# Kernel optimization log

Measured on AMD Instinct MI355X. Metric: run time of the kernel, lower is better.

## Reference

```python
import jax, jax.numpy as jnp
import numpy as np
import math

B, L, DX, DH, DFF, N, M = 16, 1024, 2, 512, 2048, 3, 8
DK = DH // M  # 64
EPS = 1e-5


def batchnorm_pos(z):
    # fresh nn.BatchNorm1d(L, affine=False) in train mode on [B, L, DH]:
    # per-position (dim 1) mean/var over (batch, feature) axes, biased variance
    mu = jnp.mean(z, axis=(0, 2), keepdims=True)
    var = jnp.mean(jnp.square(z - mu), axis=(0, 2), keepdims=True)
    return (z - mu) / jnp.sqrt(var + EPS)


def setup_inputs() -> dict:
    key = jax.random.key(0)
    ks = jax.random.split(key, 13)
    s = lambda k, shape, scale: jax.random.normal(k, shape, dtype=jnp.float32) * scale
    return {
        "x": s(ks[0], (B, L, DX), 1.0),
        "Wh": s(ks[1], (DH, DX), 1.0 / math.sqrt(DX)),
        "bh": s(ks[2], (DH,), 0.02),
        "Wq": s(ks[3], (N, M, DK, DH), 1.0 / math.sqrt(DH)),
        "Wk": s(ks[4], (N, M, DK, DH), 1.0 / math.sqrt(DH)),
        "Wv": s(ks[5], (N, M, DK, DH), 1.0 / math.sqrt(DH)),
        "Wo": s(ks[6], (N, M, DH, DK), 1.0 / math.sqrt(DK)),
        "w_bn": s(ks[7], (N, DH), 1.0),
        "b_bn": s(ks[8], (N, DH), 1.0),
        "Wff0": s(ks[9], (N, DFF, DH), 1.0 / math.sqrt(DH)),
        "bff0": s(ks[10], (N, DFF), 0.02),
        "Wff1": s(ks[11], (N, DH, DFF), 1.0 / math.sqrt(DFF)),
        "bff1": s(ks[12], (N, DH), 0.02),
    }


def reference(x, Wh, bh, Wq, Wk, Wv, Wo, w_bn, b_bn, Wff0, bff0, Wff1, bff1):
    n_layers = Wq.shape[0]
    dk = Wq.shape[2]
    scale = 1.0 / math.sqrt(dk)
    h = jnp.einsum("bld,ed->ble", x, Wh) + bh  # [B, L, DH]
    for n in range(n_layers):
        # batched multi-head attention (replaces per-head python loop)
        q = jnp.einsum("bld,mkd->bmlk", h, Wq[n])  # [B, M, L, DK]
        k = jnp.einsum("bld,mkd->bmlk", h, Wk[n])
        v = jnp.einsum("bld,mvd->bmlv", h, Wv[n])
        scores = jnp.einsum("bmlk,bmjk->bmlj", q, k) * scale  # [B, M, L, L]
        attn = jax.nn.softmax(scores, axis=-1)
        t = jnp.einsum("bmlj,bmjv->bmlv", attn, v)
        h_mha = jnp.einsum("bmlv,mdv->bld", t, Wo[n])  # sum over heads
        h_bn = w_bn[n] * batchnorm_pos(h + h_mha) + b_bn[n]
        ff = jnp.einsum("blf,df->bld", jax.nn.relu(jnp.einsum("bld,fd->blf", h_bn, Wff0[n]) + bff0[n]), Wff1[n]) + bff1[n]
        h = w_bn[n] * batchnorm_pos(h_bn + ff) + b_bn[n]
    return h
```

## Files before the change

### kernel.cpp

```cpp
#include <hip/hip_runtime.h>
#include <hip/hip_bf16.h>
#include <math.h>

#define B_   16
#define L_   1024
#define BL_  16384
#define DH_  512
#define DFF_ 2048
#define NL_  3
#define M_   8
#define DK_  64

typedef __attribute__((ext_vector_type(8))) short bf16x8;
typedef __attribute__((ext_vector_type(4))) float f32x4;
typedef __attribute__((ext_vector_type(4))) unsigned short us4;
typedef __attribute__((ext_vector_type(8))) unsigned short us8;

__device__ __forceinline__ unsigned short f2b(float x) {
    __hip_bfloat16 h = __float2bfloat16(x);
    return *(unsigned short*)&h;
}
__device__ __forceinline__ float b2f(unsigned short u) {
    unsigned int v = ((unsigned int)u) << 16;
    return __builtin_bit_cast(float, v);
}

#define GLDS(g, l) __builtin_amdgcn_global_load_lds( \
        (const __attribute__((address_space(1))) unsigned int*)(const void*)(g), \
        (__attribute__((address_space(3))) unsigned int*)(void*)(l), 16, 0, 0)

#define QKV_T 2359296
#define WO_T  786432
#define FF_T  3145728
__global__ __launch_bounds__(256) void wprep_kernel(
    const float* __restrict__ Wq, const float* __restrict__ Wk,
    const float* __restrict__ Wv, const float* __restrict__ Wo,
    const float* __restrict__ Wff0, const float* __restrict__ Wff1,
    unsigned short* __restrict__ wqkvb3, unsigned short* __restrict__ wob3,
    unsigned short* __restrict__ wff0b3, unsigned short* __restrict__ wff1b3)
{
    int i4 = (blockIdx.x * 256 + threadIdx.x) * 4;
    const float* src;
    unsigned short* dst;
    if (i4 < QKV_T) {
        int n = i4 / 786432, r = i4 % 786432;
        if (r < 262144)      src = Wq + (size_t)n * 262144 + r;
        else if (r < 524288) src = Wk + (size_t)n * 262144 + r - 262144;
        else                 src = Wv + (size_t)n * 262144 + r - 524288;
        dst = wqkvb3 + i4;
    } else if (i4 < QKV_T + WO_T) {
        int i = i4 - QKV_T;
        int n = i / 262144, r = i % 262144;
        int d = r >> 9, mv = r & 511, mm = mv >> 6, vv = mv & 63;
        src = Wo + (size_t)n * 262144 + ((size_t)mm * 512 + d) * 64 + vv;
        dst = wob3 + i;
    } else if (i4 < QKV_T + WO_T + FF_T) {
        int i = i4 - QKV_T - WO_T;
        src = Wff0 + i;
        dst = wff0b3 + i;
    } else {
        int i = i4 - QKV_T - WO_T - FF_T;
        src = Wff1 + i;
        dst = wff1b3 + i;
    }
    float4 v = *(const float4*)src;
    us4 o;
    o.x = f2b(v.x); o.y = f2b(v.y); o.z = f2b(v.z); o.w = f2b(v.w);
    *(us4*)dst = o;
}

__global__ __launch_bounds__(256) void embed_kernel(
    const float* __restrict__ x, const float* __restrict__ Wh,
    const float* __restrict__ bh, unsigned short* __restrict__ hb)
{
    int idx = blockIdx.x * 256 + threadIdx.x;
    int bl = idx >> 7;
    int e0 = (idx & 127) * 4;
    float x0 = x[bl * 2], x1 = x[bl * 2 + 1];
    us4 o;
    #pragma unroll
    for (int r = 0; r < 4; ++r) {
        int e = e0 + r;
        float v = fmaf(x0, Wh[e * 2], fmaf(x1, Wh[e * 2 + 1], bh[e]));
        ((unsigned short*)&o)[r] = f2b(v);
    }
    *(us4*)&hb[(size_t)bl * DH_ + e0] = o;
}

template<int NF>
__global__ __launch_bounds__(512, 2) void gemm8p_kernel(
    const unsigned short* __restrict__ A, const unsigned short* __restrict__ Bm,
    const float* __restrict__ bias, unsigned short* __restrict__ Cb,
    unsigned short* __restrict__ vT, int K, int cn, int flags)
{
    constexpr int BN   = NF * 64;
    constexpr int SLOT = 32768 + BN * 128;
    __shared__ unsigned char lds[2 * SLOT];

    const int tid  = threadIdx.x;
    const int lane = tid & 63, wid = tid >> 6;
    const int wr = wid >> 2, wc = wid & 3;
    const int fr = lane & 15, fq = lane >> 4;
    const int bm0 = blockIdx.y * 256, bn0 = blockIdx.x * BN;
    const int cxor = (fr & 7) << 4;

    const int srow  = tid >> 3;
    const int scole = ((tid & 7) ^ (srow & 7)) * 8;
    const unsigned short* Ag = A  + (size_t)(bm0 + srow) * K + scole;
    const unsigned short* Bg = Bm + (size_t)(bn0 + srow) * K + scole;

    f32x4 acc[8][NF];
    #pragma unroll
    for (int i = 0; i < 8; ++i)
        #pragma unroll
        for (int j = 0; j < NF; ++j)
            acc[i][j] = (f32x4){0.f, 0.f, 0.f, 0.f};

    auto ldsA = [&](int slot, int sweep) -> void* {
        return (void*)(lds + slot * SLOT + sweep * 8192 + wid * 1024);
    };
    auto ldsB = [&](int slot, int sweep) -> void* {
        return (void*)(lds + slot * SLOT + 32768 + sweep * 8192 + wid * 1024);
    };
    auto srcA = [&](int kt, int sweep) {
        return Ag + (size_t)sweep * 64 * K + kt * 64;
    };
    auto srcB = [&](int kt, int sweep) {
        return Bg + (size_t)sweep * 64 * K + kt * 64;
    };

    const int nt = K >> 6;

    if constexpr (NF == 4) {
        GLDS(srcB(0, 0), ldsB(0, 0)); GLDS(srcB(0, 1), ldsB(0, 1));
        GLDS(srcB(0, 2), ldsB(0, 2)); GLDS(srcB(0, 3), ldsB(0, 3));
    } else {
        GLDS(srcB(0, 0), ldsB(0, 0)); GLDS(srcB(0, 1), ldsB(0, 1));
    }
    GLDS(srcA(0, 0), ldsA(0, 0)); GLDS(srcA(0, 2), ldsA(0, 2));
    GLDS(srcA(0, 1), ldsA(0, 1)); GLDS(srcA(0, 3), ldsA(0, 3));
    asm volatile("s_waitcnt vmcnt(2)" ::: "memory");
    __builtin_amdgcn_s_barrier();

    for (int kt = 0; kt < nt; ++kt) {
        const int slot = kt & 1;
        const unsigned char* sb = lds + slot * SLOT;
        const int ns = slot ^ 1;
        const bool stg = (kt + 1 < nt);
        const int kn = kt + 1;

#define PHASE(P)                                                               \
    {                                                                          \
        constexpr int mh = (P) >> 1, nh = (P) & 1;                             \
        bf16x8 af[4][2], bfr[NF / 2][2];                                       \
        _Pragma("unroll")                                                      \
        for (int mi = 0; mi < 4; ++mi)                                         \
            _Pragma("unroll")                                                  \
            for (int kk = 0; kk < 2; ++kk)                                     \
                af[mi][kk] = *(const bf16x8*)(sb +                             \
                    (wr * 128 + mh * 64 + mi * 16 + fr) * 128 +                \
                    ((kk * 64 + fq * 16) ^ cxor));                             \
        _Pragma("unroll")                                                      \
        for (int ni = 0; ni < NF / 2; ++ni)                                    \
            _Pragma("unroll")                                                  \
            for (int kk = 0; kk < 2; ++kk)                                     \
                bfr[ni][kk] = *(const bf16x8*)(sb + 32768 +                    \
                    (wc * NF * 16 + nh * (NF / 2) * 16 + ni * 16 + fr) * 128 + \
                    ((kk * 64 + fq * 16) ^ cxor));                             \
        if (stg) {                                                             \
            if constexpr (NF == 4) {                                           \
                if ((P) == 0) { GLDS(srcB(kn, 0), ldsB(ns, 0));                \
                                GLDS(srcB(kn, 1), ldsB(ns, 1)); }              \
                if ((P) == 1) { GLDS(srcB(kn, 2), ldsB(ns, 2));                \
                                GLDS(srcB(kn, 3), ldsB(ns, 3)); }              \
                if ((P) == 2) { GLDS(srcA(kn, 0), ldsA(ns, 0));                \
                                GLDS(srcA(kn, 2), ldsA(ns, 2)); }              \
                if ((P) == 3) { GLDS(srcA(kn, 1), ldsA(ns, 1));                \
                                GLDS(srcA(kn, 3), ldsA(ns, 3)); }              \
            } else {                                                           \
                if ((P) == 0) { GLDS(srcB(kn, 0), ldsB(ns, 0));                \
                                GLDS(srcB(kn, 1), ldsB(ns, 1)); }              \
                if ((P) == 1) { GLDS(srcA(kn, 0), ldsA(ns, 0));                \
                                GLDS(srcA(kn, 2), ldsA(ns, 2)); }              \
                if ((P) == 2) { GLDS(srcA(kn, 1), ldsA(ns, 1));                \
                                GLDS(srcA(kn, 3), ldsA(ns, 3)); }              \
            }                                                                  \
        }                                                                      \
        if ((P) == 1) {                                                        \
            if (stg) asm volatile("s_waitcnt vmcnt(4)" ::: "memory");          \
            else     asm volatile("s_waitcnt vmcnt(0)" ::: "memory");          \
        }                                                                      \
        if ((P) == 3 && stg) asm volatile("s_waitcnt vmcnt(2)" ::: "memory");  \
        __builtin_amdgcn_s_barrier();                                          \
        asm volatile("s_waitcnt lgkmcnt(0)" ::: "memory");                     \
        __builtin_amdgcn_s_setprio(1);                                         \
        _Pragma("unroll")                                                      \
        for (int mi = 0; mi < 4; ++mi)                                         \
            _Pragma("unroll")                                                  \
            for (int ni = 0; ni < NF / 2; ++ni) {                              \
                f32x4 c = acc[mh * 4 + mi][nh * (NF / 2) + ni];                \
                c = __builtin_amdgcn_mfma_f32_16x16x32_bf16(                   \
                        af[mi][0], bfr[ni][0], c, 0, 0, 0);                    \
                c = __builtin_amdgcn_mfma_f32_16x16x32_bf16(                   \
                        af[mi][1], bfr[ni][1], c, 0, 0, 0);                    \
                acc[mh * 4 + mi][nh * (NF / 2) + ni] = c;                      \
            }                                                                  \
        __builtin_amdgcn_s_setprio(0);                                         \
        __builtin_amdgcn_s_barrier();                                          \
    }
        PHASE(0) PHASE(1) PHASE(2) PHASE(3)
#undef PHASE
    }

    float bj[NF];
    #pragma unroll
    for (int an = 0; an < NF; ++an) bj[an] = 0.f;
    if (flags & 1) {
        #pragma unroll
        for (int an = 0; an < NF; ++an)
            bj[an] = bias[bn0 + wc * NF * 16 + an * 16 + fr];
    }
    bool relu = flags & 2;
    bool qkvm = flags & 4;
    #pragma unroll
    for (int am = 0; am < 8; ++am) {
        int row0 = bm0 + wr * 128 + (am >> 2) * 64 + (am & 3) * 16 + fq * 4;
        #pragma unroll
        for (int an = 0; an < NF; ++an) {
            int col = bn0 + wc * NF * 16 + an * 16 + fr;
            float v[4];
            #pragma unroll
            for (int r = 0; r < 4; ++r) {
                v[r] = acc[am][an][r] + bj[an];
                if (relu) v[r] = fmaxf(v[r], 0.f);
            }
            if (qkvm) {
                if (col < 1024) {
                    float sc = (col < 512) ? 0.1803368801111244f : 1.0f;
                    #pragma unroll
                    for (int r = 0; r < 4; ++r)
                        Cb[(size_t)(row0 + r) * cn + col] = f2b(v[r] * sc);
                } else {
                    int mm = (col - 1024) >> 6, dd = (col - 1024) & 63;
                    int bb = row0 >> 10, l0 = row0 & 1023;
                    us4 p;
                    p.x = f2b(v[0]); p.y = f2b(v[1]); p.z = f2b(v[2]); p.w = f2b(v[3]);
                    *(us4*)&vT[((size_t)(bb * 8 + mm) * 64 + dd) * 1024 + l0] = p;
                }
            } else {
                #pragma unroll
                for (int r = 0; r < 4; ++r)
                    Cb[(size_t)(row0 + r) * cn + col] = f2b(v[r]);
            }
        }
    }
}

#define KST 72
__global__ __launch_bounds__(256, 4) void attn_mfma_kernel(
    const unsigned short* __restrict__ qk, const unsigned short* __restrict__ vT,
    unsigned short* __restrict__ t)
{
    __shared__ unsigned short Ks[64 * KST];
    __shared__ unsigned short Vs[64 * KST];
    __shared__ unsigned short Pb[4][32 * KST];

    int tid = threadIdx.x;
    int lane = tid & 63, wid = tid >> 6;
    int fr = lane & 15, fq = lane >> 4;
    int j = blockIdx.x;
    int pair = (j & 7) * 16 + (j >> 6);
    int q0 = ((j >> 3) & 7) * 128;
    int b = pair >> 3, m = pair & 7;
    int bq = b * L_;

    size_t qbase = (size_t)(bq + q0 + wid * 32) * 1024 + m * 64;
    bf16x8 qa[2][2];
    #pragma unroll
    for (int qh = 0; qh < 2; ++qh) {
        qa[qh][0] = *(const bf16x8*)&qk[qbase + (size_t)(qh * 16 + fr) * 1024 + fq * 8];
        qa[qh][1] = *(const bf16x8*)&qk[qbase + (size_t)(qh * 16 + fr) * 1024 + 32 + fq * 8];
    }

    f32x4 oacc[2][4];
    #pragma unroll
    for (int qh = 0; qh < 2; ++qh)
        #pragma unroll
        for (int i = 0; i < 4; ++i) oacc[qh][i] = (f32x4){0.f, 0.f, 0.f, 0.f};
    float lsum[2][4] = {{0.f, 0.f, 0.f, 0.f}, {0.f, 0.f, 0.f, 0.f}};

    int srow = tid >> 3;
    int scol = (tid & 7) * 8;
    const unsigned short* kg = qk + (size_t)bq * 1024 + 512 + m * 64 + scol;
    const unsigned short* vg = vT + ((size_t)pair * 64) * 1024 + scol;
    unsigned short* pw = Pb[wid];

    uint4 k0 = *(const uint4*)&kg[(size_t)(srow) * 1024];
    uint4 k1 = *(const uint4*)&kg[(size_t)(srow + 32) * 1024];
    uint4 v0 = *(const uint4*)&vg[(size_t)(srow) * 1024];
    uint4 v1 = *(const uint4*)&vg[(size_t)(srow + 32) * 1024];

    for (int kt = 0; kt < L_ / 64; ++kt) {
        __syncthreads();
        *(uint4*)&Ks[(srow)      * KST + scol] = k0;
        *(uint4*)&Ks[(srow + 32) * KST + scol] = k1;
        *(uint4*)&Vs[(srow)      * KST + scol] = v0;
        *(uint4*)&Vs[(srow + 32) * KST + scol] = v1;
        __syncthreads();
        if (kt + 1 < L_ / 64) {
            int kb = (kt + 1) * 64;
            k0 = *(const uint4*)&kg[(size_t)(kb + srow) * 1024];
            k1 = *(const uint4*)&kg[(size_t)(kb + srow + 32) * 1024];
            v0 = *(const uint4*)&vg[(size_t)(srow) * 1024 + kb];
            v1 = *(const uint4*)&vg[(size_t)(srow + 32) * 1024 + kb];
        }

        __builtin_amdgcn_s_setprio(1);
        #pragma unroll
        for (int nk = 0; nk < 4; ++nk) {
            bf16x8 kf0 = *(const bf16x8*)&Ks[(nk * 16 + fr) * KST + fq * 8];
            bf16x8 kf1 = *(const bf16x8*)&Ks[(nk * 16 + fr) * KST + 32 + fq * 8];
            #pragma unroll
            for (int qh = 0; qh < 2; ++qh) {
                f32x4 s = __builtin_amdgcn_mfma_f32_16x16x32_bf16(
                    qa[qh][0], kf0, (f32x4){0.f, 0.f, 0.f, 0.f}, 0, 0, 0);
                s = __builtin_amdgcn_mfma_f32_16x16x32_bf16(qa[qh][1], kf1, s, 0, 0, 0);
                #pragma unroll
                for (int r = 0; r < 4; ++r) {
                    float p = exp2f(s[r]);
                    lsum[qh][r] += p;
                    pw[(qh * 16 + fq * 4 + r) * KST + nk * 16 + fr] = f2b(p);
                }
            }
        }
        bf16x8 pa[2][2];
        #pragma unroll
        for (int qh = 0; qh < 2; ++qh) {
            pa[qh][0] = *(const bf16x8*)&pw[(qh * 16 + fr) * KST + fq * 8];
            pa[qh][1] = *(const bf16x8*)&pw[(qh * 16 + fr) * KST + 32 + fq * 8];
        }
        #pragma unroll
        for (int nt = 0; nt < 4; ++nt) {
            bf16x8 vf0 = *(const bf16x8*)&Vs[(nt * 16 + fr) * KST + fq * 8];
            bf16x8 vf1 = *(const bf16x8*)&Vs[(nt * 16 + fr) * KST + 32 + fq * 8];
            #pragma unroll
            for (int qh = 0; qh < 2; ++qh) {
                oacc[qh][nt] = __builtin_amdgcn_mfma_f32_16x16x32_bf16(
                    pa[qh][0], vf0, oacc[qh][nt], 0, 0, 0);
                oacc[qh][nt] = __builtin_amdgcn_mfma_f32_16x16x32_bf16(
                    pa[qh][1], vf1, oacc[qh][nt], 0, 0, 0);
            }
        }
        __builtin_amdgcn_s_setprio(0);
    }

    #pragma unroll
    for (int qh = 0; qh < 2; ++qh)
        #pragma unroll
        for (int r = 0; r < 4; ++r) {
            float s = lsum[qh][r];
            s += __shfl_xor(s, 1); s += __shfl_xor(s, 2);
            s += __shfl_xor(s, 4); s += __shfl_xor(s, 8);
            lsum[qh][r] = 1.f / s;
        }
    #pragma unroll
    for (int qh = 0; qh < 2; ++qh)
        #pragma unroll
        for (int r = 0; r < 4; ++r) {
            size_t orow = (size_t)(bq + q0 + wid * 32 + qh * 16 + fq * 4 + r) * DH_ + m * 64;
            #pragma unroll
            for (int nt = 0; nt < 4; ++nt)
                t[orow + nt * 16 + fr] = f2b(oacc[qh][nt][r] * lsum[qh][r]);
        }
}

__global__ __launch_bounds__(256) void bn_stats_kernel(
    const unsigned short* __restrict__ a, const unsigned short* __restrict__ b,
    float* __restrict__ stats)
{
    int l = blockIdx.x, tid = threadIdx.x;
    float s = 0.f, s2 = 0.f;
    #pragma unroll
    for (int u = tid; u < 1024; u += 256) {
        int bb = u >> 6, dg = (u & 63) * 8;
        size_t off = ((size_t)bb * L_ + l) * DH_ + dg;
        us8 va = *(const us8*)&a[off];
        us8 vb = *(const us8*)&b[off];
        #pragma unroll
        for (int j = 0; j < 8; ++j) {
            float z = b2f(va[j]) + b2f(vb[j]);
            s += z;
            s2 = fmaf(z, z, s2);
        }
    }
    #pragma unroll
    for (int off = 32; off > 0; off >>= 1) {
        s  += __shfl_down(s, off);
        s2 += __shfl_down(s2, off);
    }
    __shared__ float red[8];
    int w = tid >> 6;
    if ((tid & 63) == 0) { red[w] = s; red[4 + w] = s2; }
    __syncthreads();
    if (tid == 0) {
        float S  = red[0] + red[1] + red[2] + red[3];
        float S2 = red[4] + red[5] + red[6] + red[7];
        float mu  = S * (1.f / 8192.f);
        float var = S2 * (1.f / 8192.f) - mu * mu;
        stats[l]      = mu;
        stats[L_ + l] = rsqrtf(var + 1e-5f);
    }
}

__global__ __launch_bounds__(256) void bn_apply_kernel(
    const unsigned short* __restrict__ a, const unsigned short* __restrict__ b,
    const float* __restrict__ stats, const float* __restrict__ w,
    const float* __restrict__ bias, unsigned short* __restrict__ outb,
    float* __restrict__ outf)
{
    int idx = blockIdx.x * 256 + threadIdx.x;
    int bl = idx >> 6;
    int d0 = (idx & 63) * 8;
    int l  = bl & (L_ - 1);
    float mu = stats[l], rs = stats[L_ + l];
    size_t off = (size_t)bl * DH_ + d0;
    us8 va = *(const us8*)&a[off];
    us8 vb = *(const us8*)&b[off];
    float o[8];
    #pragma unroll
    for (int j = 0; j < 8; ++j) {
        float z = b2f(va[j]) + b2f(vb[j]);
        o[j] = fmaf(w[d0 + j], (z - mu) * rs, bias[d0 + j]);
    }
    if (outb) {
        us8 ob;
        #pragma unroll
        for (int j = 0; j < 8; ++j) ob[j] = f2b(o[j]);
        *(us8*)&outb[off] = ob;
    }
    if (outf) {
        float4 o0 = {o[0], o[1], o[2], o[3]};
        float4 o1 = {o[4], o[5], o[6], o[7]};
        *(float4*)&outf[off]     = o0;
        *(float4*)&outf[off + 4] = o1;
    }
}

extern "C" void kernel_launch(void* const* d_in, const int* in_sizes, int n_in,
                              void* d_out, int out_size, void* d_ws, size_t ws_size,
                              hipStream_t stream)
{
    const float* x    = (const float*)d_in[0];
    const float* Wh   = (const float*)d_in[1];
    const float* bh   = (const float*)d_in[2];
    const float* Wq   = (const float*)d_in[3];
    const float* Wk   = (const float*)d_in[4];
    const float* Wv   = (const float*)d_in[5];
    const float* Wo   = (const float*)d_in[6];
    const float* wbn  = (const float*)d_in[7];
    const float* bbn  = (const float*)d_in[8];
    const float* Wff0 = (const float*)d_in[9];
    const float* bff0 = (const float*)d_in[10];
    const float* Wff1 = (const float*)d_in[11];
    const float* bff1 = (const float*)d_in[12];
    float* out = (float*)d_out;

    float* st = (float*)d_ws;
    unsigned short* hb    = (unsigned short*)(st + 2048);
    unsigned short* qkkb  = hb + (size_t)BL_ * DH_;
    unsigned short* vTb   = qkkb + (size_t)BL_ * 1024;
    unsigned short* tb    = vTb + (size_t)BL_ * DH_;
    unsigned short* mhab  = tb + (size_t)BL_ * DH_;
    unsigned short* hbnb  = mhab + (size_t)BL_ * DH_;
    unsigned short* ffob  = hbnb + (size_t)BL_ * DH_;
    unsigned short* wqkvb3 = ffob + (size_t)BL_ * DH_;
    unsigned short* wob3   = wqkvb3 + QKV_T;
    unsigned short* wff0b3 = wob3 + WO_T;
    unsigned short* wff1b3 = wff0b3 + FF_T;
    unsigned short* ffmb  = qkkb;

    wprep_kernel<<<(QKV_T + WO_T + 2 * FF_T) / 1024, 256, 0, stream>>>(
        Wq, Wk, Wv, Wo, Wff0, Wff1, wqkvb3, wob3, wff0b3, wff1b3);
    embed_kernel<<<BL_ * DH_ / 4 / 256, 256, 0, stream>>>(x, Wh, bh, hb);

    dim3 gqkv(1536 / 128, BL_ / 256);
    dim3 gwo(512 / 128, BL_ / 256);
    dim3 gff0(2048 / 256, BL_ / 256);
    dim3 gff1(512 / 128, BL_ / 256);
    int gbn = BL_ * DH_ / 8 / 256;

    for (int n = 0; n < NL_; ++n) {
        const unsigned short* wqkvb = wqkvb3 + (size_t)n * 786432;
        const unsigned short* wob   = wob3   + (size_t)n * 262144;
        const unsigned short* wff0b = wff0b3 + (size_t)n * 1048576;
        const unsigned short* wff1b = wff1b3 + (size_t)n * 1048576;
        const float* wbn_n  = wbn  + (size_t)n * DH_;
        const float* bbn_n  = bbn  + (size_t)n * DH_;
        const float* bff0_n = bff0 + (size_t)n * DFF_;
        const float* bff1_n = bff1 + (size_t)n * DH_;
        bool last = (n == NL_ - 1);

        gemm8p_kernel<2><<<gqkv, 512, 0, stream>>>(hb, wqkvb, nullptr,
            qkkb, vTb, DH_, 1024, 4);
        attn_mfma_kernel<<<1024, 256, 0, stream>>>(qkkb, vTb, tb);
        gemm8p_kernel<2><<<gwo, 512, 0, stream>>>(tb, wob, nullptr,
            mhab, nullptr, DH_, DH_, 0);
        bn_stats_kernel<<<L_, 256, 0, stream>>>(hb, mhab, st);
        bn_apply_kernel<<<gbn, 256, 0, stream>>>(hb, mhab, st, wbn_n, bbn_n,
            hbnb, nullptr);
        gemm8p_kernel<4><<<gff0, 512, 0, stream>>>(hbnb, wff0b, bff0_n,
            ffmb, nullptr, DH_, DFF_, 1 | 2);
        gemm8p_kernel<2><<<gff1, 512, 0, stream>>>(ffmb, wff1b, bff1_n,
            ffob, nullptr, DFF_, DH_, 1);
        bn_stats_kernel<<<L_, 256, 0, stream>>>(hbnb, ffob, st);
        bn_apply_kernel<<<gbn, 256, 0, stream>>>(hbnb, ffob, st, wbn_n, bbn_n,
            last ? nullptr : hb, last ? out : nullptr);
    }
}
```

Measured before the change: 776.2 us.

## Swizzle GEMM workgroup order across XCDs and use two-phase loop for NF=2

Launches the GEMMs on a flat 1D grid and remaps each workgroup id so consecutive tiles land on the same XCD (chunked by 8). This improves L2 reuse of A and B tiles within each XCD. For NF=2 it also replaces the four-phase inner loop, whose last phases issued no loads, with a two-phase loop that spreads the next-tile global-to-LDS copies over both phases and adjusts the vmcnt waits to match. The remap relies on the grid size being divisible by 8, and the new wait counts must stay consistent with the issue order.

```diff
diff --git a/kernel.cpp b/kernel.cpp
--- a/kernel.cpp
+++ b/kernel.cpp
@@ -91,7 +91,7 @@
 __global__ __launch_bounds__(512, 2) void gemm8p_kernel(
     const unsigned short* __restrict__ A, const unsigned short* __restrict__ Bm,
     const float* __restrict__ bias, unsigned short* __restrict__ Cb,
-    unsigned short* __restrict__ vT, int K, int cn, int flags)
+    unsigned short* __restrict__ vT, int K, int cn, int flags, int gx)
 {
     constexpr int BN   = NF * 64;
     constexpr int SLOT = 32768 + BN * 128;
@@ -101,7 +101,14 @@
     const int lane = tid & 63, wid = tid >> 6;
     const int wr = wid >> 2, wc = wid & 3;
     const int fr = lane & 15, fq = lane >> 4;
-    const int bm0 = blockIdx.y * 256, bn0 = blockIdx.x * BN;
+
+    const int nwg = gridDim.x;
+    const int cpx = nwg >> 3;
+    const int wg  = blockIdx.x;
+    const int swz = (wg & 7) * cpx + (wg >> 3);
+    const int by  = swz / gx;
+    const int bx  = swz - by * gx;
+    const int bm0 = by * 256, bn0 = bx * BN;
     const int cxor = (fr & 7) << 4;
 
     const int srow  = tid >> 3;
@@ -149,10 +156,10 @@
         const bool stg = (kt + 1 < nt);
         const int kn = kt + 1;
 
-#define PHASE(P)                                                               \
+#define PHASE4(P)                                                              \
     {                                                                          \
         constexpr int mh = (P) >> 1, nh = (P) & 1;                             \
-        bf16x8 af[4][2], bfr[NF / 2][2];                                       \
+        bf16x8 af[4][2], bfr[2][2];                                            \
         _Pragma("unroll")                                                      \
         for (int mi = 0; mi < 4; ++mi)                                         \
             _Pragma("unroll")                                                  \
@@ -161,30 +168,21 @@
                     (wr * 128 + mh * 64 + mi * 16 + fr) * 128 +                \
                     ((kk * 64 + fq * 16) ^ cxor));                             \
         _Pragma("unroll")                                                      \
-        for (int ni = 0; ni < NF / 2; ++ni)                                    \
+        for (int ni = 0; ni < 2; ++ni)                                         \
             _Pragma("unroll")                                                  \
             for (int kk = 0; kk < 2; ++kk)                                     \
                 bfr[ni][kk] = *(const bf16x8*)(sb + 32768 +                    \
-                    (wc * NF * 16 + nh * (NF / 2) * 16 + ni * 16 + fr) * 128 + \
+                    (wc * 64 + nh * 32 + ni * 16 + fr) * 128 +                 \
                     ((kk * 64 + fq * 16) ^ cxor));                             \
         if (stg) {                                                             \
-            if constexpr (NF == 4) {                                           \
-                if ((P) == 0) { GLDS(srcB(kn, 0), ldsB(ns, 0));                \
-                                GLDS(srcB(kn, 1), ldsB(ns, 1)); }              \
-                if ((P) == 1) { GLDS(srcB(kn, 2), ldsB(ns, 2));                \
-                                GLDS(srcB(kn, 3), ldsB(ns, 3)); }              \
-                if ((P) == 2) { GLDS(srcA(kn, 0), ldsA(ns, 0));                \
-                                GLDS(srcA(kn, 2), ldsA(ns, 2)); }              \
-                if ((P) == 3) { GLDS(srcA(kn, 1), ldsA(ns, 1));                \
-                                GLDS(srcA(kn, 3), ldsA(ns, 3)); }              \
-            } else {                                                           \
-                if ((P) == 0) { GLDS(srcB(kn, 0), ldsB(ns, 0));                \
-                                GLDS(srcB(kn, 1), ldsB(ns, 1)); }              \
-                if ((P) == 1) { GLDS(srcA(kn, 0), ldsA(ns, 0));                \
-                                GLDS(srcA(kn, 2), ldsA(ns, 2)); }              \
-                if ((P) == 2) { GLDS(srcA(kn, 1), ldsA(ns, 1));                \
-                                GLDS(srcA(kn, 3), ldsA(ns, 3)); }              \
-            }                                                                  \
+            if ((P) == 0) { GLDS(srcB(kn, 0), ldsB(ns, 0));                    \
+                            GLDS(srcB(kn, 1), ldsB(ns, 1)); }                  \
+            if ((P) == 1) { GLDS(srcB(kn, 2), ldsB(ns, 2));                    \
+                            GLDS(srcB(kn, 3), ldsB(ns, 3)); }                  \
+            if ((P) == 2) { GLDS(srcA(kn, 0), ldsA(ns, 0));                    \
+                            GLDS(srcA(kn, 2), ldsA(ns, 2)); }                  \
+            if ((P) == 3) { GLDS(srcA(kn, 1), ldsA(ns, 1));                    \
+                            GLDS(srcA(kn, 3), ldsA(ns, 3)); }                  \
         }                                                                      \
         if ((P) == 1) {                                                        \
             if (stg) asm volatile("s_waitcnt vmcnt(4)" ::: "memory");          \
@@ -197,19 +195,74 @@
         _Pragma("unroll")                                                      \
         for (int mi = 0; mi < 4; ++mi)                                         \
             _Pragma("unroll")                                                  \
-            for (int ni = 0; ni < NF / 2; ++ni) {                              \
-                f32x4 c = acc[mh * 4 + mi][nh * (NF / 2) + ni];                \
+            for (int ni = 0; ni < 2; ++ni) {                                   \
+                f32x4 c = acc[mh * 4 + mi][nh * 2 + ni];                       \
                 c = __builtin_amdgcn_mfma_f32_16x16x32_bf16(                   \
                         af[mi][0], bfr[ni][0], c, 0, 0, 0);                    \
                 c = __builtin_amdgcn_mfma_f32_16x16x32_bf16(                   \
                         af[mi][1], bfr[ni][1], c, 0, 0, 0);                    \
-                acc[mh * 4 + mi][nh * (NF / 2) + ni] = c;                      \
+                acc[mh * 4 + mi][nh * 2 + ni] = c;                             \
             }                                                                  \
         __builtin_amdgcn_s_setprio(0);                                         \
         __builtin_amdgcn_s_barrier();                                          \
     }
-        PHASE(0) PHASE(1) PHASE(2) PHASE(3)
-#undef PHASE
+
+#define PHASE2(P)                                                              \
+    {                                                                          \
+        constexpr int mh = (P);                                                \
+        bf16x8 af[4][2], bfr[2][2];                                            \
+        _Pragma("unroll")                                                      \
+        for (int mi = 0; mi < 4; ++mi)                                         \
+            _Pragma("unroll")                                                  \
+            for (int kk = 0; kk < 2; ++kk)                                     \
+                af[mi][kk] = *(const bf16x8*)(sb +                             \
+                    (wr * 128 + mh * 64 + mi * 16 + fr) * 128 +                \
+                    ((kk * 64 + fq * 16) ^ cxor));                             \
+        _Pragma("unroll")                                                      \
+        for (int ni = 0; ni < 2; ++ni)                                         \
+            _Pragma("unroll")                                                  \
+            for (int kk = 0; kk < 2; ++kk)                                     \
+                bfr[ni][kk] = *(const bf16x8*)(sb + 32768 +                    \
+                    (wc * 32 + ni * 16 + fr) * 128 +                           \
+                    ((kk * 64 + fq * 16) ^ cxor));                             \
+        if (stg) {                                                             \
+            if ((P) == 0) { GLDS(srcB(kn, 0), ldsB(ns, 0));                    \
+                            GLDS(srcB(kn, 1), ldsB(ns, 1));                    \
+                            GLDS(srcA(kn, 0), ldsA(ns, 0)); }                  \
+            if ((P) == 1) { GLDS(srcA(kn, 2), ldsA(ns, 2));                    \
+                            GLDS(srcA(kn, 1), ldsA(ns, 1));                    \
+                            GLDS(srcA(kn, 3), ldsA(ns, 3)); }                  \
+        }                                                                      \
+        if ((P) == 0) {                                                        \
+            if (stg) asm volatile("s_waitcnt vmcnt(3)" ::: "memory");          \
+            else     asm volatile("s_waitcnt vmcnt(0)" ::: "memory");          \
+        }                                                                      \
+        if ((P) == 1 && stg) asm volatile("s_waitcnt vmcnt(2)" ::: "memory");  \
+        __builtin_amdgcn_s_barrier();                                          \
+        asm volatile("s_waitcnt lgkmcnt(0)" ::: "memory");                     \
+        __builtin_amdgcn_s_setprio(1);                                         \
+        _Pragma("unroll")                                                      \
+        for (int mi = 0; mi < 4; ++mi)                                         \
+            _Pragma("unroll")                                                  \
+            for (int ni = 0; ni < 2; ++ni) {                                   \
+                f32x4 c = acc[mh * 4 + mi][ni];                                \
+                c = __builtin_amdgcn_mfma_f32_16x16x32_bf16(                   \
+                        af[mi][0], bfr[ni][0], c, 0, 0, 0);                    \
+                c = __builtin_amdgcn_mfma_f32_16x16x32_bf16(                   \
+                        af[mi][1], bfr[ni][1], c, 0, 0, 0);                    \
+                acc[mh * 4 + mi][ni] = c;                                      \
+            }                                                                  \
+        __builtin_amdgcn_s_setprio(0);                                         \
+        __builtin_amdgcn_s_barrier();                                          \
+    }
+
+        if constexpr (NF == 4) {
+            PHASE4(0) PHASE4(1) PHASE4(2) PHASE4(3)
+        } else {
+            PHASE2(0) PHASE2(1)
+        }
+#undef PHASE4
+#undef PHASE2
     }
 
     float bj[NF];
@@ -483,10 +536,10 @@
         Wq, Wk, Wv, Wo, Wff0, Wff1, wqkvb3, wob3, wff0b3, wff1b3);
     embed_kernel<<<BL_ * DH_ / 4 / 256, 256, 0, stream>>>(x, Wh, bh, hb);
 
-    dim3 gqkv(1536 / 128, BL_ / 256);
-    dim3 gwo(512 / 128, BL_ / 256);
-    dim3 gff0(2048 / 256, BL_ / 256);
-    dim3 gff1(512 / 128, BL_ / 256);
+    const int GQKV = 12 * 64;
+    const int GWO  = 4 * 64;
+    const int GFF0 = 8 * 64;
+    const int GFF1 = 4 * 64;
     int gbn = BL_ * DH_ / 8 / 256;
 
     for (int n = 0; n < NL_; ++n) {
@@ -500,18 +553,18 @@
         const float* bff1_n = bff1 + (size_t)n * DH_;
         bool last = (n == NL_ - 1);
 
-        gemm8p_kernel<2><<<gqkv, 512, 0, stream>>>(hb, wqkvb, nullptr,
-            qkkb, vTb, DH_, 1024, 4);
+        gemm8p_kernel<2><<<GQKV, 512, 0, stream>>>(hb, wqkvb, nullptr,
+            qkkb, vTb, DH_, 1024, 4, 12);
         attn_mfma_kernel<<<1024, 256, 0, stream>>>(qkkb, vTb, tb);
-        gemm8p_kernel<2><<<gwo, 512, 0, stream>>>(tb, wob, nullptr,
-            mhab, nullptr, DH_, DH_, 0);
+        gemm8p_kernel<2><<<GWO, 512, 0, stream>>>(tb, wob, nullptr,
+            mhab, nullptr, DH_, DH_, 0, 4);
         bn_stats_kernel<<<L_, 256, 0, stream>>>(hb, mhab, st);
         bn_apply_kernel<<<gbn, 256, 0, stream>>>(hb, mhab, st, wbn_n, bbn_n,
             hbnb, nullptr);
-        gemm8p_kernel<4><<<gff0, 512, 0, stream>>>(hbnb, wff0b, bff0_n,
-            ffmb, nullptr, DH_, DFF_, 1 | 2);
-        gemm8p_kernel<2><<<gff1, 512, 0, stream>>>(ffmb, wff1b, bff1_n,
-            ffob, nullptr, DFF_, DH_, 1);
+        gemm8p_kernel<4><<<GFF0, 512, 0, stream>>>(hbnb, wff0b, bff0_n,
+            ffmb, nullptr, DH_, DFF_, 1 | 2, 8);
+        gemm8p_kernel<2><<<GFF1, 512, 0, stream>>>(ffmb, wff1b, bff1_n,
+            ffob, nullptr, DFF_, DH_, 1, 4);
         bn_stats_kernel<<<L_, 256, 0, stream>>>(hbnb, ffob, st);
         bn_apply_kernel<<<gbn, 256, 0, stream>>>(hbnb, ffob, st, wbn_n, bbn_n,
             last ? nullptr : hb, last ? out : nullptr);
```

Measured after the change: 753.6 us. 2.9% less time.

## Replace 256-row GEMM tiles with 128x128 tiles, XCD-swizzled 1D grid

Applied to the files above, without the earlier changes.

Swaps the templated 256xBN GEMM, with its four-phase barrier pipeline, for a smaller 128x128 tile kernel. The new kernel uses 64 KB of LDS and launch bounds of 4 blocks per CU, so more blocks are resident and occupancy is higher. The grid becomes one-dimensional, and block indices are swizzled across the 8 XCDs so that neighbouring tiles share L2. The cost is less data reuse per block, more global traffic, and a simpler single-barrier loop that overlaps memory and compute less.

```diff
diff --git a/kernel.cpp b/kernel.cpp
--- a/kernel.cpp
+++ b/kernel.cpp
@@ -87,21 +87,26 @@
     *(us4*)&hb[(size_t)bl * DH_ + e0] = o;
 }
 
-template<int NF>
-__global__ __launch_bounds__(512, 2) void gemm8p_kernel(
+__global__ __launch_bounds__(512, 4) void gemm2w_kernel(
     const unsigned short* __restrict__ A, const unsigned short* __restrict__ Bm,
     const float* __restrict__ bias, unsigned short* __restrict__ Cb,
-    unsigned short* __restrict__ vT, int K, int cn, int flags)
-{
-    constexpr int BN   = NF * 64;
-    constexpr int SLOT = 32768 + BN * 128;
+    unsigned short* __restrict__ vT, int K, int cn, int flags, int gx)
+{
+    constexpr int SLOT = 32768;
     __shared__ unsigned char lds[2 * SLOT];
 
     const int tid  = threadIdx.x;
     const int lane = tid & 63, wid = tid >> 6;
     const int wr = wid >> 2, wc = wid & 3;
     const int fr = lane & 15, fq = lane >> 4;
-    const int bm0 = blockIdx.y * 256, bn0 = blockIdx.x * BN;
+
+    const int nwg = gridDim.x;
+    const int cpx = nwg >> 3;
+    const int wg  = blockIdx.x;
+    const int swz = (wg & 7) * cpx + (wg >> 3);
+    const int by  = swz / gx;
+    const int bx  = swz - by * gx;
+    const int bm0 = by * 128, bn0 = bx * 128;
     const int cxor = (fr & 7) << 4;
 
     const int srow  = tid >> 3;
@@ -109,18 +114,18 @@
     const unsigned short* Ag = A  + (size_t)(bm0 + srow) * K + scole;
     const unsigned short* Bg = Bm + (size_t)(bn0 + srow) * K + scole;
 
-    f32x4 acc[8][NF];
-    #pragma unroll
-    for (int i = 0; i < 8; ++i)
-        #pragma unroll
-        for (int j = 0; j < NF; ++j)
+    f32x4 acc[4][2];
+    #pragma unroll
+    for (int i = 0; i < 4; ++i)
+        #pragma unroll
+        for (int j = 0; j < 2; ++j)
             acc[i][j] = (f32x4){0.f, 0.f, 0.f, 0.f};
 
     auto ldsA = [&](int slot, int sweep) -> void* {
         return (void*)(lds + slot * SLOT + sweep * 8192 + wid * 1024);
     };
     auto ldsB = [&](int slot, int sweep) -> void* {
-        return (void*)(lds + slot * SLOT + 32768 + sweep * 8192 + wid * 1024);
+        return (void*)(lds + slot * SLOT + 16384 + sweep * 8192 + wid * 1024);
     };
     auto srcA = [&](int kt, int sweep) {
         return Ag + (size_t)sweep * 64 * K + kt * 64;
@@ -131,15 +136,9 @@
 
     const int nt = K >> 6;
 
-    if constexpr (NF == 4) {
-        GLDS(srcB(0, 0), ldsB(0, 0)); GLDS(srcB(0, 1), ldsB(0, 1));
-        GLDS(srcB(0, 2), ldsB(0, 2)); GLDS(srcB(0, 3), ldsB(0, 3));
-    } else {
-        GLDS(srcB(0, 0), ldsB(0, 0)); GLDS(srcB(0, 1), ldsB(0, 1));
-    }
-    GLDS(srcA(0, 0), ldsA(0, 0)); GLDS(srcA(0, 2), ldsA(0, 2));
-    GLDS(srcA(0, 1), ldsA(0, 1)); GLDS(srcA(0, 3), ldsA(0, 3));
-    asm volatile("s_waitcnt vmcnt(2)" ::: "memory");
+    GLDS(srcB(0, 0), ldsB(0, 0)); GLDS(srcB(0, 1), ldsB(0, 1));
+    GLDS(srcA(0, 0), ldsA(0, 0)); GLDS(srcA(0, 1), ldsA(0, 1));
+    asm volatile("s_waitcnt vmcnt(0)" ::: "memory");
     __builtin_amdgcn_s_barrier();
 
     for (int kt = 0; kt < nt; ++kt) {
@@ -149,85 +148,65 @@
         const bool stg = (kt + 1 < nt);
         const int kn = kt + 1;
 
-#define PHASE(P)                                                               \
-    {                                                                          \
-        constexpr int mh = (P) >> 1, nh = (P) & 1;                             \
-        bf16x8 af[4][2], bfr[NF / 2][2];                                       \
-        _Pragma("unroll")                                                      \
-        for (int mi = 0; mi < 4; ++mi)                                         \
-            _Pragma("unroll")                                                  \
-            for (int kk = 0; kk < 2; ++kk)                                     \
-                af[mi][kk] = *(const bf16x8*)(sb +                             \
-                    (wr * 128 + mh * 64 + mi * 16 + fr) * 128 +                \
-                    ((kk * 64 + fq * 16) ^ cxor));                             \
-        _Pragma("unroll")                                                      \
-        for (int ni = 0; ni < NF / 2; ++ni)                                    \
-            _Pragma("unroll")                                                  \
-            for (int kk = 0; kk < 2; ++kk)                                     \
-                bfr[ni][kk] = *(const bf16x8*)(sb + 32768 +                    \
-                    (wc * NF * 16 + nh * (NF / 2) * 16 + ni * 16 + fr) * 128 + \
-                    ((kk * 64 + fq * 16) ^ cxor));                             \
-        if (stg) {                                                             \
-            if constexpr (NF == 4) {                                           \
-                if ((P) == 0) { GLDS(srcB(kn, 0), ldsB(ns, 0));                \
-                                GLDS(srcB(kn, 1), ldsB(ns, 1)); }              \
-                if ((P) == 1) { GLDS(srcB(kn, 2), ldsB(ns, 2));                \
-                                GLDS(srcB(kn, 3), ldsB(ns, 3)); }              \
-                if ((P) == 2) { GLDS(srcA(kn, 0), ldsA(ns, 0));                \
-                                GLDS(srcA(kn, 2), ldsA(ns, 2)); }              \
-                if ((P) == 3) { GLDS(srcA(kn, 1), ldsA(ns, 1));                \
-                                GLDS(srcA(kn, 3), ldsA(ns, 3)); }              \
-            } else {                                                           \
-                if ((P) == 0) { GLDS(srcB(kn, 0), ldsB(ns, 0));                \
-                                GLDS(srcB(kn, 1), ldsB(ns, 1)); }              \
-                if ((P) == 1) { GLDS(srcA(kn, 0), ldsA(ns, 0));                \
-                                GLDS(srcA(kn, 2), ldsA(ns, 2)); }              \
-                if ((P) == 2) { GLDS(srcA(kn, 1), ldsA(ns, 1));                \
-                                GLDS(srcA(kn, 3), ldsA(ns, 3)); }              \
-            }                                                                  \
-        }                                                                      \
-        if ((P) == 1) {                                                        \
-            if (stg) asm volatile("s_waitcnt vmcnt(4)" ::: "memory");          \
-            else     asm volatile("s_waitcnt vmcnt(0)" ::: "memory");          \
-        }                                                                      \
-        if ((P) == 3 && stg) asm volatile("s_waitcnt vmcnt(2)" ::: "memory");  \
-        __builtin_amdgcn_s_barrier();                                          \
-        asm volatile("s_waitcnt lgkmcnt(0)" ::: "memory");                     \
-        __builtin_amdgcn_s_setprio(1);                                         \
-        _Pragma("unroll")                                                      \
-        for (int mi = 0; mi < 4; ++mi)                                         \
-            _Pragma("unroll")                                                  \
-            for (int ni = 0; ni < NF / 2; ++ni) {                              \
-                f32x4 c = acc[mh * 4 + mi][nh * (NF / 2) + ni];                \
-                c = __builtin_amdgcn_mfma_f32_16x16x32_bf16(                   \
-                        af[mi][0], bfr[ni][0], c, 0, 0, 0);                    \
-                c = __builtin_amdgcn_mfma_f32_16x16x32_bf16(                   \
-                        af[mi][1], bfr[ni][1], c, 0, 0, 0);                    \
-                acc[mh * 4 + mi][nh * (NF / 2) + ni] = c;                      \
-            }                                                                  \
-        __builtin_amdgcn_s_setprio(0);                                         \
-        __builtin_amdgcn_s_barrier();                                          \
-    }
-        PHASE(0) PHASE(1) PHASE(2) PHASE(3)
-#undef PHASE
-    }
-
-    float bj[NF];
-    #pragma unroll
-    for (int an = 0; an < NF; ++an) bj[an] = 0.f;
+        bf16x8 bfr[2][2], af[2][2];
+        #pragma unroll
+        for (int ni = 0; ni < 2; ++ni)
+            #pragma unroll
+            for (int kk = 0; kk < 2; ++kk)
+                bfr[ni][kk] = *(const bf16x8*)(sb + 16384 +
+                    (wc * 32 + ni * 16 + fr) * 128 + ((kk * 64 + fq * 16) ^ cxor));
+        #pragma unroll
+        for (int mi = 0; mi < 2; ++mi)
+            #pragma unroll
+            for (int kk = 0; kk < 2; ++kk)
+                af[mi][kk] = *(const bf16x8*)(sb +
+                    (wr * 64 + mi * 16 + fr) * 128 + ((kk * 64 + fq * 16) ^ cxor));
+        if (stg) {
+            GLDS(srcB(kn, 0), ldsB(ns, 0)); GLDS(srcB(kn, 1), ldsB(ns, 1));
+            GLDS(srcA(kn, 0), ldsA(ns, 0)); GLDS(srcA(kn, 1), ldsA(ns, 1));
+        }
+        #pragma unroll
+        for (int mi = 0; mi < 2; ++mi)
+            #pragma unroll
+            for (int ni = 0; ni < 2; ++ni) {
+                f32x4 c = acc[mi][ni];
+                c = __builtin_amdgcn_mfma_f32_16x16x32_bf16(af[mi][0], bfr[ni][0], c, 0, 0, 0);
+                c = __builtin_amdgcn_mfma_f32_16x16x32_bf16(af[mi][1], bfr[ni][1], c, 0, 0, 0);
+                acc[mi][ni] = c;
+            }
+        #pragma unroll
+        for (int mi = 0; mi < 2; ++mi)
+            #pragma unroll
+            for (int kk = 0; kk < 2; ++kk)
+                af[mi][kk] = *(const bf16x8*)(sb +
+                    (wr * 64 + 32 + mi * 16 + fr) * 128 + ((kk * 64 + fq * 16) ^ cxor));
+        #pragma unroll
+        for (int mi = 0; mi < 2; ++mi)
+            #pragma unroll
+            for (int ni = 0; ni < 2; ++ni) {
+                f32x4 c = acc[2 + mi][ni];
+                c = __builtin_amdgcn_mfma_f32_16x16x32_bf16(af[mi][0], bfr[ni][0], c, 0, 0, 0);
+                c = __builtin_amdgcn_mfma_f32_16x16x32_bf16(af[mi][1], bfr[ni][1], c, 0, 0, 0);
+                acc[2 + mi][ni] = c;
+            }
+        if (stg) asm volatile("s_waitcnt vmcnt(0)" ::: "memory");
+        __builtin_amdgcn_s_barrier();
+    }
+
+    float bj[2] = {0.f, 0.f};
     if (flags & 1) {
         #pragma unroll
-        for (int an = 0; an < NF; ++an)
-            bj[an] = bias[bn0 + wc * NF * 16 + an * 16 + fr];
+        for (int ni = 0; ni < 2; ++ni)
+            bj[ni] = bias[bn0 + wc * 32 + ni * 16 + fr];
     }
     bool relu = flags & 2;
     bool qkvm = flags & 4;
     #pragma unroll
-    for (int am = 0; am < 8; ++am) {
-        int row0 = bm0 + wr * 128 + (am >> 2) * 64 + (am & 3) * 16 + fq * 4;
-        #pragma unroll
-        for (int an = 0; an < NF; ++an) {
-            int col = bn0 + wc * NF * 16 + an * 16 + fr;
+    for (int am = 0; am < 4; ++am) {
+        int row0 = bm0 + wr * 64 + (am >> 1) * 32 + (am & 1) * 16 + fq * 4;
+        #pragma unroll
+        for (int an = 0; an < 2; ++an) {
+            int col = bn0 + wc * 32 + an * 16 + fr;
             float v[4];
             #pragma unroll
             for (int r = 0; r < 4; ++r) {
@@ -483,10 +462,10 @@
         Wq, Wk, Wv, Wo, Wff0, Wff1, wqkvb3, wob3, wff0b3, wff1b3);
     embed_kernel<<<BL_ * DH_ / 4 / 256, 256, 0, stream>>>(x, Wh, bh, hb);
 
-    dim3 gqkv(1536 / 128, BL_ / 256);
-    dim3 gwo(512 / 128, BL_ / 256);
-    dim3 gff0(2048 / 256, BL_ / 256);
-    dim3 gff1(512 / 128, BL_ / 256);
+    const int GQKV = 12 * 128;
+    const int GWO  = 4 * 128;
+    const int GFF0 = 16 * 128;
+    const int GFF1 = 4 * 128;
     int gbn = BL_ * DH_ / 8 / 256;
 
     for (int n = 0; n < NL_; ++n) {
@@ -500,18 +479,18 @@
         const float* bff1_n = bff1 + (size_t)n * DH_;
         bool last = (n == NL_ - 1);
 
-        gemm8p_kernel<2><<<gqkv, 512, 0, stream>>>(hb, wqkvb, nullptr,
-            qkkb, vTb, DH_, 1024, 4);
+        gemm2w_kernel<<<GQKV, 512, 0, stream>>>(hb, wqkvb, nullptr,
+            qkkb, vTb, DH_, 1024, 4, 12);
         attn_mfma_kernel<<<1024, 256, 0, stream>>>(qkkb, vTb, tb);
-        gemm8p_kernel<2><<<gwo, 512, 0, stream>>>(tb, wob, nullptr,
-            mhab, nullptr, DH_, DH_, 0);
+        gemm2w_kernel<<<GWO, 512, 0, stream>>>(tb, wob, nullptr,
+            mhab, nullptr, DH_, DH_, 0, 4);
         bn_stats_kernel<<<L_, 256, 0, stream>>>(hb, mhab, st);
         bn_apply_kernel<<<gbn, 256, 0, stream>>>(hb, mhab, st, wbn_n, bbn_n,
             hbnb, nullptr);
-        gemm8p_kernel<4><<<gff0, 512, 0, stream>>>(hbnb, wff0b, bff0_n,
-            ffmb, nullptr, DH_, DFF_, 1 | 2);
-        gemm8p_kernel<2><<<gff1, 512, 0, stream>>>(ffmb, wff1b, bff1_n,
-            ffob, nullptr, DFF_, DH_, 1);
+        gemm2w_kernel<<<GFF0, 512, 0, stream>>>(hbnb, wff0b, bff0_n,
+            ffmb, nullptr, DH_, DFF_, 1 | 2, 16);
+        gemm2w_kernel<<<GFF1, 512, 0, stream>>>(ffmb, wff1b, bff1_n,
+            ffob, nullptr, DFF_, DH_, 1, 4);
         bn_stats_kernel<<<L_, 256, 0, stream>>>(hbnb, ffob, st);
         bn_apply_kernel<<<gbn, 256, 0, stream>>>(hbnb, ffob, st, wbn_n, bbn_n,
             last ? nullptr : hb, last ? out : nullptr);
```

After: 677.7 us. -12.7%, faster.
